# Optimization experiments

Hardware: AMD Instinct MI355X
Metric: run time of the kernel (lower is better)

## Reference

```python
import jax, jax.numpy as jnp
import numpy as np

B, T, E, H = 4, 2048, 1024, 16
S = E // H  # 64


def setup_inputs() -> dict:
    key = jax.random.key(0)
    ks = jax.random.split(key, 6)
    return {
        "x": jax.random.normal(ks[0], (B, T, E), dtype=jnp.float32),
        "Wk": jax.random.normal(ks[1], (S, S), dtype=jnp.float32) * (1.0 / np.sqrt(S)),
        "Wq": jax.random.normal(ks[2], (S, S), dtype=jnp.float32) * (1.0 / np.sqrt(S)),
        "Wv": jax.random.normal(ks[3], (S, S), dtype=jnp.float32) * (1.0 / np.sqrt(S)),
        "Wp": jax.random.normal(ks[4], (E, E), dtype=jnp.float32) * (1.0 / np.sqrt(E)),
        "bp": jnp.zeros((E,), dtype=jnp.float32),
    }


def reference(x, Wk, Wq, Wv, Wp, bp):
    b, t, e = x.shape
    h, s = H, S
    xh = x.reshape(b, t, h, s)
    # per-head projections share one (s,s) weight across all heads (torch Linear: y = x @ W.T)
    keys = jnp.einsum('bthi,oi->bhto', xh, Wk)     # (b,h,t,s)
    queries = jnp.einsum('bthi,oi->bhto', xh, Wq)
    values = jnp.einsum('bthi,oi->bhto', xh, Wv)
    scale = e ** 0.25  # q and k each divided by e^(1/4) -> net 1/sqrt(e)
    queries = queries / scale
    keys = keys / scale
    dot = jnp.einsum('bhqs,bhks->bhqk', queries, keys)  # (b,h,t,t)
    attn = jax.nn.softmax(dot, axis=-1)
    out = jnp.einsum('bhqk,bhks->bqhs', attn, values)   # (b,t,h,s)
    out = out.reshape(b, t, h * s)
    return jnp.einsum('bte,oe->bto', out, Wp) + bp
```

## Files before the change

### kernel.cpp

```cpp
#include <hip/hip_runtime.h>
#include <hip/hip_bf16.h>

#define Bv 4
#define Tv 2048
#define Ev 1024
#define Hv 16
#define Sv 64

typedef __attribute__((ext_vector_type(8))) short bf16x8;
typedef __attribute__((ext_vector_type(4))) short bf16x4;
typedef __attribute__((ext_vector_type(4))) float f32x4;

#if __has_builtin(__builtin_amdgcn_mfma_f32_16x16x16_bf16)
#define MFMA161616(a, b, c) __builtin_amdgcn_mfma_f32_16x16x16_bf16(a, b, c, 0, 0, 0)
#elif __has_builtin(__builtin_amdgcn_mfma_f32_16x16x16bf16_1k)
#define MFMA161616(a, b, c) __builtin_amdgcn_mfma_f32_16x16x16bf16_1k(a, b, c, 0, 0, 0)
#else
__device__ __forceinline__ f32x4 mfma161616_asm(bf16x4 a, bf16x4 b, f32x4 c) {
    f32x4 d;
    asm("v_mfma_f32_16x16x16_bf16 %0, %1, %2, %3" : "=v"(d) : "v"(a), "v"(b), "v"(c));
    return d;
}
#define MFMA161616(a, b, c) mfma161616_asm(a, b, c)
#endif

__device__ __forceinline__ ushort f2bf(float f) {
    unsigned u = __float_as_uint(f);
    u = (u + 0x7FFFu + ((u >> 16) & 1u)) >> 16;
    return (ushort)u;
}
__device__ __forceinline__ unsigned pkrn(float a, float b) {
    __hip_bfloat162 t = __float22bfloat162_rn(make_float2(a, b));
    unsigned r; __builtin_memcpy(&r, &t, 4); return r;
}
__device__ __forceinline__ unsigned pktr(float a, float b) {
    return __builtin_amdgcn_perm(__float_as_uint(b), __float_as_uint(a), 0x07060302u);
}

__device__ __forceinline__ void async16(void* lds, const void* g) {
    __builtin_amdgcn_global_load_lds(
        (const __attribute__((address_space(1))) unsigned int*)g,
        (__attribute__((address_space(3))) unsigned int*)lds, 16, 0, 0);
}

__global__ __launch_bounds__(256) void cast_kernel(
    const float* __restrict__ Wp, const float* __restrict__ Wq,
    const float* __restrict__ Wk, const float* __restrict__ Wv,
    ushort* __restrict__ Wpb, ushort* __restrict__ Wqb,
    ushort* __restrict__ Wkb, ushort* __restrict__ Wvb)
{
    int blk = blockIdx.x;
    if (blk < 1024) {
        int i = (blk * 256 + threadIdx.x) * 4;
        float4 v = *(const float4*)(Wp + i);
        uint2 o = {pkrn(v.x, v.y), pkrn(v.z, v.w)};
        *(uint2*)(Wpb + i) = o;
    } else {
        int p = blk - 1024;
        const float* src = (p == 0) ? Wq : ((p == 1) ? Wk : Wv);
        ushort* dst      = (p == 0) ? Wqb : ((p == 1) ? Wkb : Wvb);
        const float scale = (p == 0) ? 0.03125f * 1.4426950408889634f : 1.0f;
        #pragma unroll
        for (int it = 0; it < 4; ++it) {
            int i = (it * 256 + threadIdx.x) * 4;
            float4 v = *(const float4*)(src + i);
            uint2 o = {pkrn(v.x * scale, v.y * scale), pkrn(v.z * scale, v.w * scale)};
            *(uint2*)(dst + i) = o;
        }
    }
}

__global__ __launch_bounds__(192) void qkv_kernel(
    const float* __restrict__ x,
    const ushort* __restrict__ Wqb, const ushort* __restrict__ Wkb,
    const ushort* __restrict__ Wvb,
    ushort* __restrict__ Q, ushort* __restrict__ K, ushort* __restrict__ Vt)
{
    const int tid  = threadIdx.x;
    const int wave = tid >> 6;
    const int lane = tid & 63;
    const int m    = lane & 15;
    const int quad = lane >> 4;

    const ushort* Wsel = (wave == 0) ? Wqb : ((wave == 1) ? Wkb : Wvb);
    bf16x8 wf[4][2];
    #pragma unroll
    for (int ot = 0; ot < 4; ++ot)
        #pragma unroll
        for (int ks = 0; ks < 2; ++ks)
            wf[ot][ks] = *(const bf16x8*)&Wsel[(ot * 16 + m) * 64 + ks * 32 + quad * 8];

    const int tt = blockIdx.x >> 2;
    const int hg = blockIdx.x & 3;
    const int g0 = tt * 16;
    const int gm = g0 + m;
    const int b  = g0 >> 11;
    const int t0 = g0 & 2047;

    #pragma unroll
    for (int hi = 0; hi < 4; ++hi) {
        const int h  = hg * 4 + hi;
        const int bh = b * Hv + h;

        bf16x8 xf[2];
        #pragma unroll
        for (int ks = 0; ks < 2; ++ks) {
            const float* src = x + (size_t)gm * Ev + h * Sv + ks * 32 + quad * 8;
            float4 v0 = *(const float4*)src;
            float4 v1 = *(const float4*)(src + 4);
            unsigned pk[4];
            pk[0] = pkrn(v0.x, v0.y); pk[1] = pkrn(v0.z, v0.w);
            pk[2] = pkrn(v1.x, v1.y); pk[3] = pkrn(v1.z, v1.w);
            xf[ks] = *(bf16x8*)pk;
        }

        f32x4 acc[4];
        #pragma unroll
        for (int ot = 0; ot < 4; ++ot) acc[ot] = (f32x4){0.f, 0.f, 0.f, 0.f};

        if (wave < 2) {
            #pragma unroll
            for (int ks = 0; ks < 2; ++ks)
                #pragma unroll
                for (int ot = 0; ot < 4; ++ot)
                    acc[ot] = __builtin_amdgcn_mfma_f32_16x16x32_bf16(
                        wf[ot][ks], xf[ks], acc[ot], 0, 0, 0);
            ushort* dst = ((wave == 0) ? Q : K)
                        + ((size_t)bh * Tv + t0 + m) * Sv + quad * 4;
            #pragma unroll
            for (int ot = 0; ot < 4; ++ot) {
                uint2 w = {pkrn(acc[ot][0], acc[ot][1]), pkrn(acc[ot][2], acc[ot][3])};
                *(uint2*)(dst + ot * 16) = w;
            }
        } else {
            #pragma unroll
            for (int ks = 0; ks < 2; ++ks)
                #pragma unroll
                for (int st = 0; st < 4; ++st)
                    acc[st] = __builtin_amdgcn_mfma_f32_16x16x32_bf16(
                        xf[ks], wf[st][ks], acc[st], 0, 0, 0);
            ushort* vr = Vt + ((size_t)bh * Sv + m) * Tv + t0 + quad * 4;
            #pragma unroll
            for (int st = 0; st < 4; ++st) {
                uint2 w = {pkrn(acc[st][0], acc[st][1]), pkrn(acc[st][2], acc[st][3])};
                *(uint2*)(vr + (size_t)st * 16 * Tv) = w;
            }
        }
    }
}

__global__ __launch_bounds__(256, 4) void attn_kernel(
    const ushort* __restrict__ Q, const ushort* __restrict__ K,
    const ushort* __restrict__ Vt, ushort* __restrict__ O)
{
    __shared__ ushort kl[64 * 64];
    __shared__ ushort vl[64 * 64];
    __shared__ float  ll[4][32];

    const int tid  = threadIdx.x;
    const int wave = tid >> 6;
    const int lane = tid & 63;
    const int m    = lane & 15;
    const int quad = lane >> 4;
    const int bh   = blockIdx.x & 63;
    const int q0   = (blockIdx.x >> 6) << 7;

    const ushort* Qb = Q + ((size_t)bh * Tv + q0 + wave * 32) * Sv;
    bf16x8 qf[2][2];
    #pragma unroll
    for (int g = 0; g < 2; ++g)
        #pragma unroll
        for (int ks = 0; ks < 2; ++ks)
            qf[g][ks] = *(const bf16x8*)&Qb[(g * 16 + m) * Sv + ks * 32 + quad * 8];

    f32x4 oa[2][4];
    float lsum[2] = {0.f, 0.f};
    #pragma unroll
    for (int g = 0; g < 2; ++g)
        #pragma unroll
        for (int st = 0; st < 4; ++st)
            oa[g][st] = (f32x4){0.f, 0.f, 0.f, 0.f};

    const ushort* Kb = K  + (size_t)bh * Tv * Sv;
    const ushort* Vb = Vt + (size_t)bh * Sv * Tv;

    const int r0 = tid >> 3,         cg0 = (tid & 7) ^ (r0 & 7);
    const int r1 = (256 + tid) >> 3, cg1 = ((256 + tid) & 7) ^ (r1 & 7);
    const size_t koff0 = (size_t)r0 * Sv + cg0 * 8;
    const size_t koff1 = (size_t)r1 * Sv + cg1 * 8;
    const size_t voff0 = (size_t)r0 * Tv + cg0 * 8;
    const size_t voff1 = (size_t)r1 * Tv + cg1 * 8;
    const int mx = m & 7;

    for (int k0 = 0; k0 < Tv; k0 += 64) {
        __syncthreads();
        async16(&kl[(size_t)tid * 8],         Kb + (size_t)k0 * Sv + koff0);
        async16(&kl[((size_t)tid + 256) * 8], Kb + (size_t)k0 * Sv + koff1);
        async16(&vl[(size_t)tid * 8],         Vb + k0 + voff0);
        async16(&vl[((size_t)tid + 256) * 8], Vb + k0 + voff1);
        __syncthreads();

        bf16x4 w[4][2];
        #pragma unroll
        for (int nt = 0; nt < 4; ++nt) {
            const int krow = nt * 16 + m;
            bf16x8 a0 = *(const bf16x8*)&kl[krow * 64 + ((quad       ^ mx) * 8)];
            bf16x8 a1 = *(const bf16x8*)&kl[krow * 64 + (((4 + quad) ^ mx) * 8)];
            #pragma unroll
            for (int g = 0; g < 2; ++g) {
                f32x4 s = (f32x4){0.f, 0.f, 0.f, 0.f};
                s = __builtin_amdgcn_mfma_f32_16x16x32_bf16(a0, qf[g][0], s, 0, 0, 0);
                s = __builtin_amdgcn_mfma_f32_16x16x32_bf16(a1, qf[g][1], s, 0, 0, 0);
                float p0 = __builtin_amdgcn_exp2f(s[0]);
                float p1 = __builtin_amdgcn_exp2f(s[1]);
                float p2 = __builtin_amdgcn_exp2f(s[2]);
                float p3 = __builtin_amdgcn_exp2f(s[3]);
                lsum[g] += (p0 + p1) + (p2 + p3);
                unsigned pk[2] = {pktr(p0, p1), pktr(p2, p3)};
                w[nt][g] = *(bf16x4*)pk;
            }
        }

        #pragma unroll
        for (int st = 0; st < 4; ++st) {
            const int srow = st * 16 + m;
            bf16x4 vf[4];
            #pragma unroll
            for (int kt = 0; kt < 4; ++kt)
                vf[kt] = *(const bf16x4*)&vl[srow * 64
                           + (((2 * kt + (quad >> 1)) ^ mx) * 8) + (quad & 1) * 4];
            #pragma unroll
            for (int g = 0; g < 2; ++g)
                #pragma unroll
                for (int kt = 0; kt < 4; ++kt)
                    oa[g][st] = MFMA161616(w[kt][g], vf[kt], oa[g][st]);
        }
    }

    #pragma unroll
    for (int g = 0; g < 2; ++g) {
        lsum[g] += __shfl_xor(lsum[g], 16, 64);
        lsum[g] += __shfl_xor(lsum[g], 32, 64);
    }
    if (lane < 16) {
        ll[wave][lane]      = 1.0f / lsum[0];
        ll[wave][16 + lane] = 1.0f / lsum[1];
    }

    const int b = bh >> 4, h = bh & 15;
    #pragma unroll
    for (int g = 0; g < 2; ++g)
        #pragma unroll
        for (int st = 0; st < 4; ++st)
            #pragma unroll
            for (int r = 0; r < 4; ++r)
                O[((size_t)(b * Tv + q0 + wave * 32 + g * 16 + quad * 4 + r)) * Ev
                  + h * Sv + st * 16 + m]
                    = f2bf(oa[g][st][r] * ll[wave][g * 16 + quad * 4 + r]);
}

__global__ __launch_bounds__(256) void proj_kernel(
    const ushort* __restrict__ A, const ushort* __restrict__ B,
    const float* __restrict__ bp, float* __restrict__ C)
{
    __shared__ ushort Asm[128 * 32];
    __shared__ ushort Bsm[128 * 32];
    const int tid  = threadIdx.x;
    const int wave = tid >> 6;
    const int lane = tid & 63;
    const int m    = lane & 15;
    const int quad = lane >> 4;
    const int wm   = wave >> 1;
    const int wn   = wave & 1;
    const int m0   = blockIdx.x * 128;
    const int n0   = blockIdx.y * 128;

    f32x4 acc[4][4];
    #pragma unroll
    for (int i = 0; i < 4; ++i)
        #pragma unroll
        for (int j = 0; j < 4; ++j)
            acc[i][j] = (f32x4){0.f, 0.f, 0.f, 0.f};

    for (int k0 = 0; k0 < Ev; k0 += 32) {
        __syncthreads();
        #pragma unroll
        for (int j = 0; j < 2; ++j) {
            int c   = j * 256 + tid;
            int row = c >> 2;
            int col = (c & 3) * 8;
            async16(&Asm[c * 8], &A[(size_t)(m0 + row) * Ev + k0 + col]);
            async16(&Bsm[c * 8], &B[(size_t)(n0 + row) * Ev + k0 + col]);
        }
        __syncthreads();

        bf16x8 af[4], bf[4];
        #pragma unroll
        for (int i = 0; i < 4; ++i)
            af[i] = *(const bf16x8*)&Asm[(wm * 64 + i * 16 + m) * 32 + quad * 8];
        #pragma unroll
        for (int j = 0; j < 4; ++j)
            bf[j] = *(const bf16x8*)&Bsm[(wn * 64 + j * 16 + m) * 32 + quad * 8];
        #pragma unroll
        for (int i = 0; i < 4; ++i)
            #pragma unroll
            for (int j = 0; j < 4; ++j)
                acc[i][j] = __builtin_amdgcn_mfma_f32_16x16x32_bf16(
                    af[i], bf[j], acc[i][j], 0, 0, 0);
    }

    float bbv[4];
    #pragma unroll
    for (int j = 0; j < 4; ++j)
        bbv[j] = bp[n0 + wn * 64 + j * 16 + m];

    #pragma unroll
    for (int i = 0; i < 4; ++i)
        #pragma unroll
        for (int j = 0; j < 4; ++j)
            #pragma unroll
            for (int r = 0; r < 4; ++r)
                C[(size_t)(m0 + wm * 64 + i * 16 + quad * 4 + r) * Ev
                  + n0 + wn * 64 + j * 16 + m] = acc[i][j][r] + bbv[j];
}

extern "C" void kernel_launch(void* const* d_in, const int* in_sizes, int n_in,
                              void* d_out, int out_size, void* d_ws, size_t ws_size,
                              hipStream_t stream) {
    const float* x  = (const float*)d_in[0];
    const float* Wk = (const float*)d_in[1];
    const float* Wq = (const float*)d_in[2];
    const float* Wv = (const float*)d_in[3];
    const float* Wp = (const float*)d_in[4];
    const float* bp = (const float*)d_in[5];
    float* out = (float*)d_out;

    ushort* Q   = (ushort*)d_ws;
    ushort* K   = Q   + 8388608;
    ushort* Vt  = K   + 8388608;
    ushort* O   = Vt  + 8388608;
    ushort* Wpb = O   + 8388608;
    ushort* Wqb = Wpb + 1048576;
    ushort* Wkb = Wqb + 4096;
    ushort* Wvb = Wkb + 4096;

    cast_kernel<<<1027, 256, 0, stream>>>(Wp, Wq, Wk, Wv, Wpb, Wqb, Wkb, Wvb);
    qkv_kernel<<<2048, 192, 0, stream>>>(x, Wqb, Wkb, Wvb, Q, K, Vt);
    attn_kernel<<<1024, 256, 0, stream>>>(Q, K, Vt, O);
    proj_kernel<<<dim3(64, 8), 256, 0, stream>>>(O, Wpb, bp, out);
}
```

Measured before the change: 224.4 us.

## Double-buffer K/V and GEMM operand tiles in shared memory with prefetch

Both the attention kernel and the output-projection GEMM now keep two shared-memory buffers for their streamed tiles. Each iteration starts the async loads for the next tile before computing on the current one, so global-memory latency overlaps with MFMA work. This also drops one of the two barriers per iteration. In exchange, shared-memory use per block doubles, which may limit how many blocks fit on a compute unit.

```diff
diff --git a/kernel.cpp b/kernel.cpp
--- a/kernel.cpp
+++ b/kernel.cpp
@@ -153,8 +153,8 @@
     const ushort* __restrict__ Q, const ushort* __restrict__ K,
     const ushort* __restrict__ Vt, ushort* __restrict__ O)
 {
-    __shared__ ushort kl[64 * 64];
-    __shared__ ushort vl[64 * 64];
+    __shared__ ushort kl[2][64 * 64];
+    __shared__ ushort vl[2][64 * 64];
     __shared__ float  ll[4][32];
 
     const int tid  = threadIdx.x;
@@ -192,20 +192,30 @@
     const size_t voff1 = (size_t)r1 * Tv + cg1 * 8;
     const int mx = m & 7;
 
-    for (int k0 = 0; k0 < Tv; k0 += 64) {
+    async16(&kl[0][(size_t)tid * 8],         Kb + koff0);
+    async16(&kl[0][((size_t)tid + 256) * 8], Kb + koff1);
+    async16(&vl[0][(size_t)tid * 8],         Vb + voff0);
+    async16(&vl[0][((size_t)tid + 256) * 8], Vb + voff1);
+
+    for (int t = 0; t < Tv / 64; ++t) {
+        const int cur = t & 1;
         __syncthreads();
-        async16(&kl[(size_t)tid * 8],         Kb + (size_t)k0 * Sv + koff0);
-        async16(&kl[((size_t)tid + 256) * 8], Kb + (size_t)k0 * Sv + koff1);
-        async16(&vl[(size_t)tid * 8],         Vb + k0 + voff0);
-        async16(&vl[((size_t)tid + 256) * 8], Vb + k0 + voff1);
-        __syncthreads();
+
+        if (t + 1 < Tv / 64) {
+            const int nxt = cur ^ 1;
+            const size_t k0n = (size_t)(t + 1) * 64;
+            async16(&kl[nxt][(size_t)tid * 8],         Kb + k0n * Sv + koff0);
+            async16(&kl[nxt][((size_t)tid + 256) * 8], Kb + k0n * Sv + koff1);
+            async16(&vl[nxt][(size_t)tid * 8],         Vb + k0n + voff0);
+            async16(&vl[nxt][((size_t)tid + 256) * 8], Vb + k0n + voff1);
+        }
 
         bf16x4 w[4][2];
         #pragma unroll
         for (int nt = 0; nt < 4; ++nt) {
             const int krow = nt * 16 + m;
-            bf16x8 a0 = *(const bf16x8*)&kl[krow * 64 + ((quad       ^ mx) * 8)];
-            bf16x8 a1 = *(const bf16x8*)&kl[krow * 64 + (((4 + quad) ^ mx) * 8)];
+            bf16x8 a0 = *(const bf16x8*)&kl[cur][krow * 64 + ((quad       ^ mx) * 8)];
+            bf16x8 a1 = *(const bf16x8*)&kl[cur][krow * 64 + (((4 + quad) ^ mx) * 8)];
             #pragma unroll
             for (int g = 0; g < 2; ++g) {
                 f32x4 s = (f32x4){0.f, 0.f, 0.f, 0.f};
@@ -227,7 +237,7 @@
             bf16x4 vf[4];
             #pragma unroll
             for (int kt = 0; kt < 4; ++kt)
-                vf[kt] = *(const bf16x4*)&vl[srow * 64
+                vf[kt] = *(const bf16x4*)&vl[cur][srow * 64
                            + (((2 * kt + (quad >> 1)) ^ mx) * 8) + (quad & 1) * 4];
             #pragma unroll
             for (int g = 0; g < 2; ++g)
@@ -263,8 +273,8 @@
     const ushort* __restrict__ A, const ushort* __restrict__ B,
     const float* __restrict__ bp, float* __restrict__ C)
 {
-    __shared__ ushort Asm[128 * 32];
-    __shared__ ushort Bsm[128 * 32];
+    __shared__ ushort Asm[2][128 * 32];
+    __shared__ ushort Bsm[2][128 * 32];
     const int tid  = threadIdx.x;
     const int wave = tid >> 6;
     const int lane = tid & 63;
@@ -282,25 +292,34 @@
         for (int j = 0; j < 4; ++j)
             acc[i][j] = (f32x4){0.f, 0.f, 0.f, 0.f};
 
-    for (int k0 = 0; k0 < Ev; k0 += 32) {
+    const int row_ = tid >> 2, col_ = (tid & 3) * 8;
+    const int rowh = (256 + tid) >> 2, colh = ((256 + tid) & 3) * 8;
+
+    async16(&Asm[0][(size_t)tid * 8],         &A[(size_t)(m0 + row_) * Ev + col_]);
+    async16(&Asm[0][((size_t)tid + 256) * 8], &A[(size_t)(m0 + rowh) * Ev + colh]);
+    async16(&Bsm[0][(size_t)tid * 8],         &B[(size_t)(n0 + row_) * Ev + col_]);
+    async16(&Bsm[0][((size_t)tid + 256) * 8], &B[(size_t)(n0 + rowh) * Ev + colh]);
+
+    for (int t = 0; t < Ev / 32; ++t) {
+        const int cur = t & 1;
         __syncthreads();
-        #pragma unroll
-        for (int j = 0; j < 2; ++j) {
-            int c   = j * 256 + tid;
-            int row = c >> 2;
-            int col = (c & 3) * 8;
-            async16(&Asm[c * 8], &A[(size_t)(m0 + row) * Ev + k0 + col]);
-            async16(&Bsm[c * 8], &B[(size_t)(n0 + row) * Ev + k0 + col]);
-        }
-        __syncthreads();
+
+        if (t + 1 < Ev / 32) {
+            const int nxt = cur ^ 1;
+            const int k0n = (t + 1) * 32;
+            async16(&Asm[nxt][(size_t)tid * 8],         &A[(size_t)(m0 + row_) * Ev + k0n + col_]);
+            async16(&Asm[nxt][((size_t)tid + 256) * 8], &A[(size_t)(m0 + rowh) * Ev + k0n + colh]);
+            async16(&Bsm[nxt][(size_t)tid * 8],         &B[(size_t)(n0 + row_) * Ev + k0n + col_]);
+            async16(&Bsm[nxt][((size_t)tid + 256) * 8], &B[(size_t)(n0 + rowh) * Ev + k0n + colh]);
+        }
 
         bf16x8 af[4], bf[4];
         #pragma unroll
         for (int i = 0; i < 4; ++i)
-            af[i] = *(const bf16x8*)&Asm[(wm * 64 + i * 16 + m) * 32 + quad * 8];
+            af[i] = *(const bf16x8*)&Asm[cur][(wm * 64 + i * 16 + m) * 32 + quad * 8];
         #pragma unroll
         for (int j = 0; j < 4; ++j)
-            bf[j] = *(const bf16x8*)&Bsm[(wn * 64 + j * 16 + m) * 32 + quad * 8];
+            bf[j] = *(const bf16x8*)&Bsm[cur][(wn * 64 + j * 16 + m) * 32 + quad * 8];
         #pragma unroll
         for (int i = 0; i < 4; ++i)
             #pragma unroll
```

New measurement: 229.1 us. 1.02x slower.

## Switch attention kernel to 32x32x16 MFMA tiles with permlane32 swap

Applied to the files above, without the earlier changes.

Rewrites the attention inner loop to use 32x32x16 bf16 MFMA for both QK^T and PV instead of 16x16x32/16x16x16 tiles. The S accumulator is exponentiated and repacked into the PV A-operand with v_permlane32_swap, so P stays in registers. Larger MFMA tiles mean fewer instructions and fewer LDS fragment reads per flop. The cost is higher register pressure from the 16-wide accumulators and a more intricate lane mapping for the output and row-sum scaling.

```diff
diff --git a/kernel.cpp b/kernel.cpp
--- a/kernel.cpp
+++ b/kernel.cpp
@@ -10,19 +10,7 @@
 typedef __attribute__((ext_vector_type(8))) short bf16x8;
 typedef __attribute__((ext_vector_type(4))) short bf16x4;
 typedef __attribute__((ext_vector_type(4))) float f32x4;
-
-#if __has_builtin(__builtin_amdgcn_mfma_f32_16x16x16_bf16)
-#define MFMA161616(a, b, c) __builtin_amdgcn_mfma_f32_16x16x16_bf16(a, b, c, 0, 0, 0)
-#elif __has_builtin(__builtin_amdgcn_mfma_f32_16x16x16bf16_1k)
-#define MFMA161616(a, b, c) __builtin_amdgcn_mfma_f32_16x16x16bf16_1k(a, b, c, 0, 0, 0)
-#else
-__device__ __forceinline__ f32x4 mfma161616_asm(bf16x4 a, bf16x4 b, f32x4 c) {
-    f32x4 d;
-    asm("v_mfma_f32_16x16x16_bf16 %0, %1, %2, %3" : "=v"(d) : "v"(a), "v"(b), "v"(c));
-    return d;
-}
-#define MFMA161616(a, b, c) mfma161616_asm(a, b, c)
-#endif
+typedef __attribute__((ext_vector_type(16))) float f32x16;
 
 __device__ __forceinline__ ushort f2bf(float f) {
     unsigned u = __float_as_uint(f);
@@ -160,26 +148,24 @@
     const int tid  = threadIdx.x;
     const int wave = tid >> 6;
     const int lane = tid & 63;
-    const int m    = lane & 15;
-    const int quad = lane >> 4;
+    const int r31  = lane & 31;
+    const int hi   = lane >> 5;
     const int bh   = blockIdx.x & 63;
     const int q0   = (blockIdx.x >> 6) << 7;
 
-    const ushort* Qb = Q + ((size_t)bh * Tv + q0 + wave * 32) * Sv;
-    bf16x8 qf[2][2];
-    #pragma unroll
-    for (int g = 0; g < 2; ++g)
-        #pragma unroll
-        for (int ks = 0; ks < 2; ++ks)
-            qf[g][ks] = *(const bf16x8*)&Qb[(g * 16 + m) * Sv + ks * 32 + quad * 8];
-
-    f32x4 oa[2][4];
-    float lsum[2] = {0.f, 0.f};
-    #pragma unroll
-    for (int g = 0; g < 2; ++g)
-        #pragma unroll
-        for (int st = 0; st < 4; ++st)
-            oa[g][st] = (f32x4){0.f, 0.f, 0.f, 0.f};
+    const ushort* Qb = Q + ((size_t)bh * Tv + q0 + wave * 32 + r31) * Sv + hi * 8;
+    bf16x8 qf[4];
+    #pragma unroll
+    for (int ks = 0; ks < 4; ++ks)
+        qf[ks] = *(const bf16x8*)(Qb + ks * 16);
+
+    f32x16 oa[2];
+    #pragma unroll
+    for (int st = 0; st < 2; ++st)
+        #pragma unroll
+        for (int r = 0; r < 16; ++r)
+            oa[st][r] = 0.f;
+    float lsum = 0.f;
 
     const ushort* Kb = K  + (size_t)bh * Tv * Sv;
     const ushort* Vb = Vt + (size_t)bh * Sv * Tv;
@@ -190,7 +176,7 @@
     const size_t koff1 = (size_t)r1 * Sv + cg1 * 8;
     const size_t voff0 = (size_t)r0 * Tv + cg0 * 8;
     const size_t voff1 = (size_t)r1 * Tv + cg1 * 8;
-    const int mx = m & 7;
+    const int swz = r31 & 7;
 
     for (int k0 = 0; k0 < Tv; k0 += 64) {
         __syncthreads();
@@ -200,63 +186,67 @@
         async16(&vl[((size_t)tid + 256) * 8], Vb + k0 + voff1);
         __syncthreads();
 
-        bf16x4 w[4][2];
-        #pragma unroll
-        for (int nt = 0; nt < 4; ++nt) {
-            const int krow = nt * 16 + m;
-            bf16x8 a0 = *(const bf16x8*)&kl[krow * 64 + ((quad       ^ mx) * 8)];
-            bf16x8 a1 = *(const bf16x8*)&kl[krow * 64 + (((4 + quad) ^ mx) * 8)];
-            #pragma unroll
-            for (int g = 0; g < 2; ++g) {
-                f32x4 s = (f32x4){0.f, 0.f, 0.f, 0.f};
-                s = __builtin_amdgcn_mfma_f32_16x16x32_bf16(a0, qf[g][0], s, 0, 0, 0);
-                s = __builtin_amdgcn_mfma_f32_16x16x32_bf16(a1, qf[g][1], s, 0, 0, 0);
-                float p0 = __builtin_amdgcn_exp2f(s[0]);
-                float p1 = __builtin_amdgcn_exp2f(s[1]);
-                float p2 = __builtin_amdgcn_exp2f(s[2]);
-                float p3 = __builtin_amdgcn_exp2f(s[3]);
-                lsum[g] += (p0 + p1) + (p2 + p3);
-                unsigned pk[2] = {pktr(p0, p1), pktr(p2, p3)};
-                w[nt][g] = *(bf16x4*)pk;
+        #pragma unroll
+        for (int kt = 0; kt < 2; ++kt) {
+            f32x16 sacc;
+            #pragma unroll
+            for (int r = 0; r < 16; ++r) sacc[r] = 0.f;
+            #pragma unroll
+            for (int ks = 0; ks < 4; ++ks) {
+                bf16x8 kf = *(const bf16x8*)
+                    &kl[(kt * 32 + r31) * 64 + (((ks * 2 + hi) ^ swz) * 8)];
+                sacc = __builtin_amdgcn_mfma_f32_32x32x16_bf16(
+                    kf, qf[ks], sacc, 0, 0, 0);
             }
-        }
-
-        #pragma unroll
-        for (int st = 0; st < 4; ++st) {
-            const int srow = st * 16 + m;
-            bf16x4 vf[4];
-            #pragma unroll
-            for (int kt = 0; kt < 4; ++kt)
-                vf[kt] = *(const bf16x4*)&vl[srow * 64
-                           + (((2 * kt + (quad >> 1)) ^ mx) * 8) + (quad & 1) * 4];
-            #pragma unroll
-            for (int g = 0; g < 2; ++g)
+
+            #pragma unroll
+            for (int kp = 0; kp < 2; ++kp) {
+                float p[8];
                 #pragma unroll
-                for (int kt = 0; kt < 4; ++kt)
-                    oa[g][st] = MFMA161616(w[kt][g], vf[kt], oa[g][st]);
+                for (int j = 0; j < 8; ++j)
+                    p[j] = __builtin_amdgcn_exp2f(sacc[kp * 8 + j]);
+                lsum += ((p[0] + p[1]) + (p[2] + p[3]))
+                      + ((p[4] + p[5]) + (p[6] + p[7]));
+                unsigned d0 = pktr(p[0], p[1]);
+                unsigned d1 = pktr(p[2], p[3]);
+                unsigned d2 = pktr(p[4], p[5]);
+                unsigned d3 = pktr(p[6], p[7]);
+                asm volatile("v_permlane32_swap_b32 %0, %1"
+                             : "+v"(d0), "+v"(d2));
+                asm volatile("v_permlane32_swap_b32 %0, %1"
+                             : "+v"(d1), "+v"(d3));
+                unsigned pw[4] = {d0, d1, d2, d3};
+                bf16x8 pf = *(bf16x8*)pw;
+
+                const int kc = (kt * 2 + kp) * 2 + hi;
+                #pragma unroll
+                for (int st = 0; st < 2; ++st) {
+                    bf16x8 vf = *(const bf16x8*)
+                        &vl[(st * 32 + r31) * 64 + ((kc ^ swz) * 8)];
+                    oa[st] = __builtin_amdgcn_mfma_f32_32x32x16_bf16(
+                        pf, vf, oa[st], 0, 0, 0);
+                }
+            }
         }
     }
 
-    #pragma unroll
-    for (int g = 0; g < 2; ++g) {
-        lsum[g] += __shfl_xor(lsum[g], 16, 64);
-        lsum[g] += __shfl_xor(lsum[g], 32, 64);
-    }
-    if (lane < 16) {
-        ll[wave][lane]      = 1.0f / lsum[0];
-        ll[wave][16 + lane] = 1.0f / lsum[1];
-    }
+    lsum += __shfl_xor(lsum, 32, 64);
+    if (lane < 32) ll[wave][lane] = 1.0f / lsum;
+
+    float sc[16];
+    #pragma unroll
+    for (int r = 0; r < 16; ++r)
+        sc[r] = ll[wave][(r & 3) + 4 * hi + 8 * (r >> 2)];
 
     const int b = bh >> 4, h = bh & 15;
     #pragma unroll
-    for (int g = 0; g < 2; ++g)
-        #pragma unroll
-        for (int st = 0; st < 4; ++st)
-            #pragma unroll
-            for (int r = 0; r < 4; ++r)
-                O[((size_t)(b * Tv + q0 + wave * 32 + g * 16 + quad * 4 + r)) * Ev
-                  + h * Sv + st * 16 + m]
-                    = f2bf(oa[g][st][r] * ll[wave][g * 16 + quad * 4 + r]);
+    for (int st = 0; st < 2; ++st)
+        #pragma unroll
+        for (int r = 0; r < 16; ++r) {
+            const int q = (r & 3) + 4 * hi + 8 * (r >> 2);
+            O[((size_t)(b * Tv + q0 + wave * 32 + q)) * Ev
+              + h * Sv + st * 32 + r31] = f2bf(oa[st][r] * sc[r]);
+        }
 }
 
 __global__ __launch_bounds__(256) void proj_kernel(
```

New measurement: 222.2 us. About the same (-1.0%).
